# Kernel optimization log

Measured on AMD Instinct MI355X. Metric: run time of the kernel, lower is better.

Reference implementation:

```python
import jax, jax.numpy as jnp
import numpy as np

N, E, B = 20000, 160000, 64
NFEAT, NHID, HEADS, NCLASS = 128, 64, 16, 10
GAT_SLOPE = 0.2    # LeakyReLU inside GATv2 attention
OUT_SLOPE = 0.01   # torch.nn.functional.leaky_relu default
TEMPERATURE = 1.0


def _lrelu(x, slope):
    return jnp.where(x >= 0, x, slope * x)


def gatv2_conv(x, src, dst, Wl, bl, Wr, br, att, bias):
    # x: [N, Fin]; PyG GATv2Conv with share_weights=False, concat=False (mean over heads)
    xl = (x @ Wl + bl).reshape(N, HEADS, NHID)   # source-side transform
    xr = (x @ Wr + br).reshape(N, HEADS, NHID)   # target-side transform
    e = _lrelu(xl[src] + xr[dst], GAT_SLOPE)     # [E', H, C] per-edge pre-activation
    logit = jnp.einsum('ehc,hc->eh', e, att)     # [E', H]
    # segment softmax over incoming edges of each target node (self-loops guarantee >=1 edge)
    m = jax.ops.segment_max(logit, dst, num_segments=N)
    m = jnp.where(jnp.isfinite(m), m, 0.0)
    ex = jnp.exp(logit - m[dst])
    den = jax.ops.segment_sum(ex, dst, num_segments=N)
    alpha = ex / den[dst]                        # [E', H]
    out = jax.ops.segment_sum(alpha[:, :, None] * xl[src], dst, num_segments=N)  # [N, H, C]
    return out.mean(axis=1) + bias               # concat=False -> head average, then bias


def setup_inputs() -> dict:
    key = jax.random.key(0)
    ks = jax.random.split(key, 20)
    s = 0.05
    inp = {
        'x': jax.random.normal(ks[0], (N, NFEAT), dtype=jnp.float32),
        'edge_index': jax.random.randint(ks[1], (2, E), 0, N, dtype=jnp.int64)
            if jax.config.jax_enable_x64 else jax.random.randint(ks[1], (2, E), 0, N).astype(jnp.int32),
        'batch': jnp.sort(jax.random.randint(ks[2], (N,), 0, B)).astype(jnp.int32),
        # GATv2 layer 1
        'W1l': jax.random.normal(ks[3], (NFEAT, HEADS * NHID), dtype=jnp.float32) * s,
        'b1l': jnp.zeros((HEADS * NHID,), jnp.float32),
        'W1r': jax.random.normal(ks[4], (NFEAT, HEADS * NHID), dtype=jnp.float32) * s,
        'b1r': jnp.zeros((HEADS * NHID,), jnp.float32),
        'att1': jax.random.normal(ks[5], (HEADS, NHID), dtype=jnp.float32) * s,
        'bias1': jnp.zeros((NHID,), jnp.float32),
        # GATv2 layer 2
        'W2l': jax.random.normal(ks[6], (NHID, HEADS * NHID), dtype=jnp.float32) * s,
        'b2l': jnp.zeros((HEADS * NHID,), jnp.float32),
        'W2r': jax.random.normal(ks[7], (NHID, HEADS * NHID), dtype=jnp.float32) * s,
        'b2r': jnp.zeros((HEADS * NHID,), jnp.float32),
        'att2': jax.random.normal(ks[8], (HEADS, NHID), dtype=jnp.float32) * s,
        'bias2': jnp.zeros((NHID,), jnp.float32),
        # heads
        'Wc': jax.random.normal(ks[9], (NHID, NCLASS), dtype=jnp.float32) * s,
        'bc': jnp.zeros((NCLASS,), jnp.float32),
        'Wv': jax.random.normal(ks[10], (NHID, 1), dtype=jnp.float32) * s,
        'bv': jnp.zeros((1,), jnp.float32),
    }
    return inp


def reference(x, edge_index, batch, W1l, b1l, W1r, b1r, att1, bias1,
              W2l, b2l, W2r, b2r, att2, bias2, Wc, bc, Wv, bv):
    loop = jnp.arange(N, dtype=edge_index.dtype)  # PyG add_self_loops=True
    src = jnp.concatenate([edge_index[0], loop])
    dst = jnp.concatenate([edge_index[1], loop])

    h = _lrelu(gatv2_conv(x, src, dst, W1l, b1l, W1r, b1r, att1, bias1), OUT_SLOPE)
    h = _lrelu(gatv2_conv(h, src, dst, W2l, b2l, W2r, b2r, att2, bias2), OUT_SLOPE)
    # dropout p=0.0 -> identity

    sums = jax.ops.segment_sum(h, batch, num_segments=B)           # [B, NHID]
    cnt = jax.ops.segment_sum(jnp.ones((N,), h.dtype), batch, num_segments=B)
    pooled = sums / jnp.maximum(cnt, 1.0)[:, None]                 # global_mean_pool

    logits = (pooled @ Wc + bc) / TEMPERATURE                      # [B, NCLASS]
    log_var = pooled @ Wv + bv                                     # [B, 1]
    return (logits, log_var)
```

## Files before the change

### kernel.cpp

```cpp
#include <hip/hip_runtime.h>
#include <hip/hip_bf16.h>
#include <hip/hip_fp16.h>
#include <math.h>

#define NN   20000
#define EE   160000
#define NBAT 64
#define NF   128
#define NH   64
#define NHEAD 16
#define NCLS 10
#define ETOT (EE + NN)

typedef __attribute__((ext_vector_type(8))) _Float16 half8;
typedef __attribute__((ext_vector_type(2))) _Float16 h2v;
typedef __attribute__((ext_vector_type(4))) float f32x4;
typedef unsigned short ushort_t;

#if __has_builtin(__builtin_amdgcn_fdot2)
typedef __fp16 fdot2_t __attribute__((ext_vector_type(2)));
static __device__ __forceinline__ float dot2(h2v a, h2v b, float c) {
    return __builtin_amdgcn_fdot2(__builtin_bit_cast(fdot2_t, a),
                                  __builtin_bit_cast(fdot2_t, b), c, false);
}
#else
static __device__ __forceinline__ float dot2(h2v a, h2v b, float c) {
    return c + (float)a.x * (float)b.x + (float)a.y * (float)b.y;
}
#endif

__global__ void k_hist(const int* __restrict__ ei, int* __restrict__ deg) {
    int e = blockIdx.x * 256 + threadIdx.x;
    if (e < EE) atomicAdd(&deg[ei[EE + e]], 1);
}

__global__ void k_scan(const int* __restrict__ deg, int* __restrict__ rowptr,
                       int* __restrict__ cursor, int* __restrict__ csr) {
    const int T = 1024, PER = (NN + T - 1) / T;
    __shared__ int part[T];
    int t = threadIdx.x;
    int local[PER];
    int s = 0;
    #pragma unroll
    for (int i = 0; i < PER; ++i) {
        int idx = t * PER + i;
        int v = (idx < NN) ? deg[idx] : 0;
        local[i] = v; s += v;
    }
    part[t] = s;
    __syncthreads();
    for (int off = 1; off < T; off <<= 1) {
        int v = (t >= off) ? part[t - off] : 0;
        __syncthreads();
        part[t] += v;
        __syncthreads();
    }
    int ex = (t == 0) ? 0 : part[t - 1];
    #pragma unroll
    for (int i = 0; i < PER; ++i) {
        int idx = t * PER + i;
        if (idx < NN) {
            int base = ex + idx;
            rowptr[idx] = base;
            csr[base]   = idx;
            cursor[idx] = base + 1;
            ex += local[i];
        }
    }
    if (t == T - 1) rowptr[NN] = ex + NN;
}

__global__ void k_scatter(const int* __restrict__ ei, int* __restrict__ cursor,
                          int* __restrict__ csr) {
    int e = blockIdx.x * 256 + threadIdx.x;
    if (e >= EE) return;
    int s = ei[e], d = ei[EE + e];
    int pos = atomicAdd(&cursor[d], 1);
    csr[pos] = s;
}

__global__ void k_bounds(const int* __restrict__ batch, int* __restrict__ bstart) {
    int n = blockIdx.x * 256 + threadIdx.x;
    if (n >= NN) return;
    int b = batch[n];
    if (n == 0) for (int bb = 0; bb <= b; ++bb) bstart[bb] = 0;
    int bn = (n + 1 < NN) ? batch[n + 1] : NBAT;
    for (int bb = b + 1; bb <= bn; ++bb) bstart[bb] = n + 1;
}

__global__ void k_split_w4(
    const float* __restrict__ W0, _Float16* __restrict__ T0,
    const float* __restrict__ W1, _Float16* __restrict__ T1,
    const float* __restrict__ W2, _Float16* __restrict__ T2,
    const float* __restrict__ W3, _Float16* __restrict__ T3)
{
    const int z = blockIdx.y;
    const float* W; _Float16* T; int K;
    if      (z == 0) { W = W0; T = T0; K = NF; }
    else if (z == 1) { W = W1; T = T1; K = NF; }
    else if (z == 2) { W = W2; T = T2; K = NH; }
    else             { W = W3; T = T3; K = NH; }
    int idx = blockIdx.x * 256 + threadIdx.x;
    if (idx >= K * 1024) return;
    int k = idx >> 10, n = idx & 1023;
    T[n * K + k] = (_Float16)W[idx];
}


template<int K>
__global__ __launch_bounds__(256) void k_gemm_l1(
    const float* __restrict__ X, int M,
    const _Float16* __restrict__ Wt0, const float* __restrict__ b0, _Float16* __restrict__ O0,
    const _Float16* __restrict__ Wt1, const float* __restrict__ b1, _Float16* __restrict__ O1)
{
    const _Float16* Wt = blockIdx.z ? Wt1 : Wt0;
    const float*    bi = blockIdx.z ? b1 : b0;
    _Float16*       O  = blockIdx.z ? O1 : O0;

    const int r0 = blockIdx.x * 128;
    const int c0 = blockIdx.y * 128;

    __shared__ __align__(16) ushort_t SH[128 * 128];
    char* AsB = (char*)SH;
    char* WsB = (char*)SH + 16384;

    const int t = threadIdx.x;
    const int lane = t & 63;
    const int wv = t >> 6, wr = wv >> 1, wc = wv & 1;
    const int fr = lane & 15;
    const int k0 = (lane >> 4) * 8;

    f32x4 acc[4][4] = {};

    for (int kt = 0; kt < K; kt += 64) {
        #pragma unroll
        for (int p = 0; p < 4; ++p) {
            int idx = p * 256 + t;
            int m  = idx >> 3;
            int kc = (idx & 7) * 8;
            int gr = r0 + m;
            half8 hv = {};
            if (gr < M) {
                float4 v0 = *(const float4*)(X + (size_t)gr * K + kt + kc);
                float4 v1 = *(const float4*)(X + (size_t)gr * K + kt + kc + 4);
                hv[0] = (_Float16)v0.x; hv[1] = (_Float16)v0.y;
                hv[2] = (_Float16)v0.z; hv[3] = (_Float16)v0.w;
                hv[4] = (_Float16)v1.x; hv[5] = (_Float16)v1.y;
                hv[6] = (_Float16)v1.z; hv[7] = (_Float16)v1.w;
            }
            int sw = (m * 128 + kc * 2) ^ ((m & 7) << 4);
            *(uint4*)(AsB + sw) = __builtin_bit_cast(uint4, hv);
            uint4 wv4 = *(const uint4*)(Wt + (size_t)(c0 + m) * K + kt + kc);
            *(uint4*)(WsB + sw) = wv4;
        }
        __syncthreads();

        #pragma unroll
        for (int ks = 0; ks < 64; ks += 32) {
            half8 a[4], b[4];
            #pragma unroll
            for (int i = 0; i < 4; ++i) {
                int row = wr * 64 + i * 16 + fr;
                int off = (row * 128 + (ks + k0) * 2) ^ ((row & 7) << 4);
                a[i] = *(const half8*)(AsB + off);
            }
            #pragma unroll
            for (int j = 0; j < 4; ++j) {
                int col = wc * 64 + j * 16 + fr;
                int off = (col * 128 + (ks + k0) * 2) ^ ((col & 7) << 4);
                b[j] = *(const half8*)(WsB + off);
            }
            #pragma unroll
            for (int i = 0; i < 4; ++i)
                #pragma unroll
                for (int j = 0; j < 4; ++j)
                    acc[i][j] = __builtin_amdgcn_mfma_f32_16x16x32_f16(a[i], b[j], acc[i][j], 0, 0, 0);
        }
        __syncthreads();
    }

    float bj[4];
    #pragma unroll
    for (int j = 0; j < 4; ++j) bj[j] = bi[c0 + wc * 64 + j * 16 + fr];
    #pragma unroll
    for (int i = 0; i < 4; ++i) {
        #pragma unroll
        for (int r = 0; r < 4; ++r) {
            int row_l = wr * 64 + i * 16 + (lane >> 4) * 4 + r;
            int s = ((row_l >> 2) & 7) << 4;
            #pragma unroll
            for (int j = 0; j < 4; ++j) {
                int col_l = wc * 64 + j * 16 + fr;
                *(_Float16*)((char*)SH + ((row_l * 256 + col_l * 2) ^ s)) =
                    (_Float16)(acc[i][j][r] + bj[j]);
            }
        }
    }
    __syncthreads();
    #pragma unroll
    for (int it = 0; it < 8; ++it) {
        int idx = it * 256 + t;
        int row_l = idx >> 4, c16 = idx & 15;
        int gr = r0 + row_l;
        if (gr < M) {
            int s = ((row_l >> 2) & 7) << 4;
            uint4 v = *(const uint4*)((char*)SH + ((row_l * 256 + c16 * 16) ^ s));
            *(uint4*)(O + (size_t)gr * 1024 + c0 + c16 * 8) = v;
        }
    }
}

template<int K>
__global__ __launch_bounds__(256) void k_gemm_l2(
    const _Float16* __restrict__ A, int M,
    const _Float16* __restrict__ Wt0, const float* __restrict__ b0, _Float16* __restrict__ O0,
    const _Float16* __restrict__ Wt1, const float* __restrict__ b1, _Float16* __restrict__ O1)
{
    const _Float16* Wt = blockIdx.z ? Wt1 : Wt0;
    const float*    bi = blockIdx.z ? b1 : b0;
    _Float16*       O  = blockIdx.z ? O1 : O0;

    const int r0 = blockIdx.x * 128;
    const int c0 = blockIdx.y * 128;

    __shared__ __align__(16) ushort_t SH[128 * 128];
    char* AsB = (char*)SH;
    char* WsB = (char*)SH + 16384;

    const int t = threadIdx.x;
    const int lane = t & 63;
    const int wv = t >> 6, wr = wv >> 1, wc = wv & 1;
    const int fr = lane & 15;
    const int k0 = (lane >> 4) * 8;

    f32x4 acc[4][4] = {};

    #pragma unroll
    for (int p = 0; p < 4; ++p) {
        int idx = p * 256 + t;
        int m  = idx >> 3;
        int kc = (idx & 7) * 8;
        int gr = r0 + m;
        uint4 av = make_uint4(0, 0, 0, 0);
        if (gr < M) av = *(const uint4*)(A + (size_t)gr * K + kc);
        int sw = (m * 128 + kc * 2) ^ ((m & 7) << 4);
        *(uint4*)(AsB + sw) = av;
        uint4 wv4 = *(const uint4*)(Wt + (size_t)(c0 + m) * K + kc);
        *(uint4*)(WsB + sw) = wv4;
    }
    __syncthreads();

    #pragma unroll
    for (int ks = 0; ks < 64; ks += 32) {
        half8 a[4], b[4];
        #pragma unroll
        for (int i = 0; i < 4; ++i) {
            int row = wr * 64 + i * 16 + fr;
            int off = (row * 128 + (ks + k0) * 2) ^ ((row & 7) << 4);
            a[i] = *(const half8*)(AsB + off);
        }
        #pragma unroll
        for (int j = 0; j < 4; ++j) {
            int col = wc * 64 + j * 16 + fr;
            int off = (col * 128 + (ks + k0) * 2) ^ ((col & 7) << 4);
            b[j] = *(const half8*)(WsB + off);
        }
        #pragma unroll
        for (int i = 0; i < 4; ++i)
            #pragma unroll
            for (int j = 0; j < 4; ++j)
                acc[i][j] = __builtin_amdgcn_mfma_f32_16x16x32_f16(a[i], b[j], acc[i][j], 0, 0, 0);
    }
    __syncthreads();

    float bj[4];
    #pragma unroll
    for (int j = 0; j < 4; ++j) bj[j] = bi[c0 + wc * 64 + j * 16 + fr];
    #pragma unroll
    for (int i = 0; i < 4; ++i) {
        #pragma unroll
        for (int r = 0; r < 4; ++r) {
            int row_l = wr * 64 + i * 16 + (lane >> 4) * 4 + r;
            int s = ((row_l >> 2) & 7) << 4;
            #pragma unroll
            for (int j = 0; j < 4; ++j) {
                int col_l = wc * 64 + j * 16 + fr;
                *(_Float16*)((char*)SH + ((row_l * 256 + col_l * 2) ^ s)) =
                    (_Float16)(acc[i][j][r] + bj[j]);
            }
        }
    }
    __syncthreads();
    #pragma unroll
    for (int it = 0; it < 8; ++it) {
        int idx = it * 256 + t;
        int row_l = idx >> 4, c16 = idx & 15;
        int gr = r0 + row_l;
        if (gr < M) {
            int s = ((row_l >> 2) & 7) << 4;
            uint4 v = *(const uint4*)((char*)SH + ((row_l * 256 + c16 * 16) ^ s));
            *(uint4*)(O + (size_t)gr * 1024 + c0 + c16 * 8) = v;
        }
    }
}

static __device__ __forceinline__ float logit8(
    half8 a0, half8 a1, half8 xr0, half8 xr1, const h2v* att2)
{
    half8 t0 = a0 + xr0;
    half8 t1 = a1 + xr1;
    t0 = __builtin_elementwise_max(t0, t0 * (_Float16)0.2f);
    t1 = __builtin_elementwise_max(t1, t1 * (_Float16)0.2f);
    const h2v* p0 = (const h2v*)&t0;
    const h2v* p1 = (const h2v*)&t1;
    float lg = 0.f;
    #pragma unroll
    for (int j = 0; j < 4; ++j) lg = dot2(p0[j], att2[j], lg);
    #pragma unroll
    for (int j = 0; j < 4; ++j) lg = dot2(p1[j], att2[4 + j], lg);
    return lg;
}

template<int SPLIT>
__global__ __launch_bounds__(256) void k_attn(
    const _Float16* __restrict__ xl, const _Float16* __restrict__ xr,
    const float* __restrict__ att, const float* __restrict__ bias,
    const int* __restrict__ rowptr, const int* __restrict__ csr,
    float* __restrict__ hout, _Float16* __restrict__ h1out)
{
    const int wave = threadIdx.x >> 6;
    const int lane = threadIdx.x & 63;
    const int n = blockIdx.x * 4 + wave;
    if (n >= NN) return;
    const int h  = lane >> 2;
    const int cc = lane & 3;
    const int cb = h * NH + cc * 16;

    h2v att2[8];
    #pragma unroll
    for (int i = 0; i < 4; ++i) {
        float4 a = *(const float4*)(att + cb + i * 4);
        att2[i * 2 + 0] = h2v{(_Float16)a.x, (_Float16)a.y};
        att2[i * 2 + 1] = h2v{(_Float16)a.z, (_Float16)a.w};
    }
    const half8 xr0 = *(const half8*)(xr + (size_t)n * 1024 + cb);
    const half8 xr1 = *(const half8*)(xr + (size_t)n * 1024 + cb + 8);

    float acc[16];
    #pragma unroll
    for (int j = 0; j < 16; ++j) acc[j] = 0.f;
    float den = 0.f;

    const int e0 = rowptr[n], e1 = rowptr[n + 1];
    for (int e = e0; e < e1; e += 4) {
        int src[4];
        #pragma unroll
        for (int j = 0; j < 4; ++j) {
            int ee = e + j;
            src[j] = csr[(ee < e1) ? ee : (e1 - 1)];
        }
        half8 xa0[4], xa1[4];
        #pragma unroll
        for (int j = 0; j < 4; ++j) {
            const _Float16* p = xl + (size_t)src[j] * 1024 + cb;
            xa0[j] = *(const half8*)p;
            xa1[j] = *(const half8*)(p + 8);
        }
        #pragma unroll
        for (int j = 0; j < 4; ++j) {
            float lg = logit8(xa0[j], xa1[j], xr0, xr1, att2);
            lg += __shfl_xor(lg, 1);
            lg += __shfl_xor(lg, 2);
            float p = (e + j < e1) ? __expf(lg) : 0.f;
            den += p;
            const _Float16* va = (const _Float16*)&xa0[j];
            const _Float16* vb = (const _Float16*)&xa1[j];
            #pragma unroll
            for (int q = 0; q < 8; ++q) acc[q]     = fmaf((float)va[q], p, acc[q]);
            #pragma unroll
            for (int q = 0; q < 8; ++q) acc[8 + q] = fmaf((float)vb[q], p, acc[8 + q]);
        }
    }

    const float inv = 1.f / den;
    float v[16];
    #pragma unroll
    for (int j = 0; j < 16; ++j) v[j] = acc[j] * inv;
    #pragma unroll
    for (int mask = 4; mask <= 32; mask <<= 1)
        #pragma unroll
        for (int j = 0; j < 16; ++j) v[j] += __shfl_xor(v[j], mask);

    if (h == 0) {
        float bvv[16];
        #pragma unroll
        for (int i = 0; i < 4; ++i)
            *(float4*)(bvv + i * 4) = *(const float4*)(bias + cc * 16 + i * 4);
        float o[16];
        #pragma unroll
        for (int j = 0; j < 16; ++j) {
            float tt = v[j] * 0.0625f + bvv[j];
            o[j] = fmaxf(tt, 0.01f * tt);
        }
        if (SPLIT) {
            half8 o0, o1;
            #pragma unroll
            for (int j = 0; j < 8; ++j) { o0[j] = (_Float16)o[j]; o1[j] = (_Float16)o[8 + j]; }
            *(half8*)(h1out + (size_t)n * NH + cc * 16)     = o0;
            *(half8*)(h1out + (size_t)n * NH + cc * 16 + 8) = o1;
        } else {
            #pragma unroll
            for (int i = 0; i < 4; ++i)
                *(float4*)(hout + (size_t)n * NH + cc * 16 + i * 4) =
                    make_float4(o[i * 4], o[i * 4 + 1], o[i * 4 + 2], o[i * 4 + 3]);
        }
    }
}

#define PNODES 128
__global__ __launch_bounds__(256) void k_pool_partial(
    const float* __restrict__ h2buf, const int* __restrict__ batch,
    float* __restrict__ sums)
{
    const int n0 = blockIdx.x * PNODES;
    const int c = threadIdx.x & 63;
    const int r = threadIdx.x >> 6;
    const int nend = (n0 + PNODES < NN) ? n0 + PNODES : NN;
    float s = 0.f;
    int bcur = -1;
    for (int n = n0 + r; n < nend; n += 4) {
        int b = batch[n];
        if (b != bcur) {
            if (bcur >= 0) atomicAdd(&sums[bcur * NH + c], s);
            bcur = b; s = 0.f;
        }
        s += h2buf[(size_t)n * NH + c];
    }
    if (bcur >= 0) atomicAdd(&sums[bcur * NH + c], s);
}

__global__ void k_heads(const float* __restrict__ sums, const int* __restrict__ bstart,
                        const float* __restrict__ Wc, const float* __restrict__ bc,
                        const float* __restrict__ Wv, const float* __restrict__ bv,
                        float* __restrict__ out)
{
    const int b = blockIdx.x, c = threadIdx.x;
    const float cnt = (float)(bstart[b + 1] - bstart[b]);
    const float pooled = sums[b * NH + c] / fmaxf(cnt, 1.f);
    __shared__ float pl[NH];
    pl[c] = pooled;
    __syncthreads();
    if (c < NCLS) {
        float a = bc[c];
        for (int k = 0; k < NH; ++k) a = fmaf(pl[k], Wc[k * NCLS + c], a);
        out[b * NCLS + c] = a;
    } else if (c == NCLS) {
        float a = bv[0];
        for (int k = 0; k < NH; ++k) a = fmaf(pl[k], Wv[k], a);
        out[NBAT * NCLS + b] = a;
    }
}

extern "C" void kernel_launch(void* const* d_in, const int* in_sizes, int n_in,
                              void* d_out, int out_size, void* d_ws, size_t ws_size,
                              hipStream_t stream)
{
    const float* x     = (const float*)d_in[0];
    const int*   ei    = (const int*)  d_in[1];
    const int*   batch = (const int*)  d_in[2];
    const float* W1l = (const float*)d_in[3],  *b1l = (const float*)d_in[4];
    const float* W1r = (const float*)d_in[5],  *b1r = (const float*)d_in[6];
    const float* att1 = (const float*)d_in[7], *bias1 = (const float*)d_in[8];
    const float* W2l = (const float*)d_in[9],  *b2l = (const float*)d_in[10];
    const float* W2r = (const float*)d_in[11], *b2r = (const float*)d_in[12];
    const float* att2 = (const float*)d_in[13], *bias2 = (const float*)d_in[14];
    const float* Wc = (const float*)d_in[15],  *bc = (const float*)d_in[16];
    const float* Wv = (const float*)d_in[17],  *bv = (const float*)d_in[18];
    float* out = (float*)d_out;

    char* ws = (char*)d_ws;
    size_t off = 0;
    auto carve = [&](size_t bytes) {
        char* p = ws + off;
        off = (off + bytes + 255) & ~(size_t)255;
        return p;
    };
    _Float16* xl    = (_Float16*)carve((size_t)NN * 1024 * 2);
    _Float16* xr    = (_Float16*)carve((size_t)NN * 1024 * 2);
    float*    h2b   = (float*)carve((size_t)NN * NH * 4);
    float*    psums = (float*)carve((size_t)NBAT * NH * 4);
    _Float16* h1    = (_Float16*)carve((size_t)NN * NH * 2);
    _Float16* Wt1l  = (_Float16*)carve((size_t)1024 * NF * 2);
    _Float16* Wt1r  = (_Float16*)carve((size_t)1024 * NF * 2);
    _Float16* Wt2l  = (_Float16*)carve((size_t)1024 * NH * 2);
    _Float16* Wt2r  = (_Float16*)carve((size_t)1024 * NH * 2);
    int*      deg    = (int*)carve((size_t)NN * 4);
    int*      cursor = (int*)carve((size_t)NN * 4);
    int*      rowptr = (int*)carve((size_t)(NN + 1) * 4);
    int*      csr    = (int*)carve((size_t)ETOT * 4);
    int*      bstart = (int*)carve((size_t)(NBAT + 1) * 4);

    hipMemsetAsync(deg, 0, (size_t)NN * 4, stream);
    k_hist   <<<(EE + 255) / 256, 256, 0, stream>>>(ei, deg);
    k_scan   <<<1, 1024, 0, stream>>>(deg, rowptr, cursor, csr);
    k_scatter<<<(EE + 255) / 256, 256, 0, stream>>>(ei, cursor, csr);
    k_bounds <<<(NN + 255) / 256, 256, 0, stream>>>(batch, bstart);

    k_split_w4<<<dim3((NF * 1024 + 255) / 256, 4), 256, 0, stream>>>(
        W1l, Wt1l, W1r, Wt1r, W2l, Wt2l, W2r, Wt2r);

    const int MB = (NN + 127) / 128;
    k_gemm_l1<NF><<<dim3(MB, 8, 2), 256, 0, stream>>>(
        x, NN, Wt1l, b1l, xl, Wt1r, b1r, xr);
    k_attn<1><<<NN / 4, 256, 0, stream>>>(xl, xr, att1, bias1, rowptr, csr,
                                          (float*)nullptr, h1);
    k_gemm_l2<NH><<<dim3(MB, 8, 2), 256, 0, stream>>>(
        h1, NN, Wt2l, b2l, xl, Wt2r, b2r, xr);
    k_attn<0><<<NN / 4, 256, 0, stream>>>(xl, xr, att2, bias2, rowptr, csr,
                                          h2b, (_Float16*)nullptr);
    hipMemsetAsync(psums, 0, (size_t)NBAT * NH * 4, stream);
    k_pool_partial<<<(NN + PNODES - 1) / PNODES, 256, 0, stream>>>(h2b, batch, psums);
    k_heads<<<NBAT, NH, 0, stream>>>(psums, bstart, Wc, bc, Wv, bv, out);
}
```

Before: 357.4 us.

## Parallelize CSR scan, fuse bounds into histogram, fuse pooling into layer-2 attention

Replaces the single-block 1024-thread scan with a three-kernel multi-block scan (block scans, a serial prefix over block sums, then a final pass). Merges the batch-bounds kernel into the histogram kernel. Removes the layer-2 output buffer and the pooling kernel by having the second attention kernel atomically add each node's output straight into the per-graph sums. This trades many contended float atomics on 64x64 targets, about 20000 nodes times 64 channels, for dropping a 5 MB write/read and one launch, and it adds two scan launches.

Measured after the change: 758.1 us. +112.1%, slower.

```diff
diff --git a/kernel.cpp b/kernel.cpp
--- a/kernel.cpp
+++ b/kernel.cpp
@@ -12,6 +12,9 @@
 #define NCLS 10
 #define ETOT (EE + NN)
 
+#define SCAN_BLK 1024
+#define SCAN_NB  ((NN + SCAN_BLK - 1) / SCAN_BLK)
+
 typedef __attribute__((ext_vector_type(8))) _Float16 half8;
 typedef __attribute__((ext_vector_type(2))) _Float16 h2v;
 typedef __attribute__((ext_vector_type(4))) float f32x4;
@@ -29,45 +32,55 @@
 }
 #endif
 
-__global__ void k_hist(const int* __restrict__ ei, int* __restrict__ deg) {
-    int e = blockIdx.x * 256 + threadIdx.x;
-    if (e < EE) atomicAdd(&deg[ei[EE + e]], 1);
-}
-
-__global__ void k_scan(const int* __restrict__ deg, int* __restrict__ rowptr,
-                       int* __restrict__ cursor, int* __restrict__ csr) {
-    const int T = 1024, PER = (NN + T - 1) / T;
-    __shared__ int part[T];
-    int t = threadIdx.x;
-    int local[PER];
-    int s = 0;
-    #pragma unroll
-    for (int i = 0; i < PER; ++i) {
-        int idx = t * PER + i;
-        int v = (idx < NN) ? deg[idx] : 0;
-        local[i] = v; s += v;
-    }
-    part[t] = s;
+__global__ void k_hist_bounds(const int* __restrict__ ei, int* __restrict__ deg,
+                              const int* __restrict__ batch, int* __restrict__ bstart) {
+    int g = blockIdx.x * 256 + threadIdx.x;
+    if (g < EE) atomicAdd(&deg[ei[EE + g]], 1);
+    if (g < NN) {
+        int b = batch[g];
+        if (g == 0) for (int bb = 0; bb <= b; ++bb) bstart[bb] = 0;
+        int bn = (g + 1 < NN) ? batch[g + 1] : NBAT;
+        for (int bb = b + 1; bb <= bn; ++bb) bstart[bb] = g + 1;
+    }
+}
+
+__global__ void k_scanA(const int* __restrict__ deg, int* __restrict__ incl,
+                        int* __restrict__ bsum) {
+    __shared__ int sh[SCAN_BLK];
+    int t = threadIdx.x, idx = blockIdx.x * SCAN_BLK + t;
+    int v = (idx < NN) ? deg[idx] : 0;
+    sh[t] = v;
     __syncthreads();
-    for (int off = 1; off < T; off <<= 1) {
-        int v = (t >= off) ? part[t - off] : 0;
+    for (int off = 1; off < SCAN_BLK; off <<= 1) {
+        int u = (t >= off) ? sh[t - off] : 0;
         __syncthreads();
-        part[t] += v;
+        sh[t] += u;
         __syncthreads();
     }
-    int ex = (t == 0) ? 0 : part[t - 1];
-    #pragma unroll
-    for (int i = 0; i < PER; ++i) {
-        int idx = t * PER + i;
-        if (idx < NN) {
-            int base = ex + idx;
-            rowptr[idx] = base;
-            csr[base]   = idx;
-            cursor[idx] = base + 1;
-            ex += local[i];
-        }
-    }
-    if (t == T - 1) rowptr[NN] = ex + NN;
+    incl[idx] = sh[t];
+    if (t == SCAN_BLK - 1) bsum[blockIdx.x] = sh[t];
+}
+
+__global__ void k_scanB(const int* __restrict__ bsum, int* __restrict__ boff,
+                        int* __restrict__ rowptr) {
+    if (threadIdx.x == 0) {
+        int acc = 0;
+        for (int b = 0; b < SCAN_NB; ++b) { boff[b] = acc; acc += bsum[b]; }
+        rowptr[NN] = acc + NN;
+    }
+}
+
+__global__ void k_scanC(const int* __restrict__ deg, const int* __restrict__ incl,
+                        const int* __restrict__ boff, int* __restrict__ rowptr,
+                        int* __restrict__ cursor, int* __restrict__ csr) {
+    int idx = blockIdx.x * 256 + threadIdx.x;
+    if (idx >= NN) return;
+    int b = idx >> 10;
+    int excl = boff[b] + incl[idx] - deg[idx];
+    int base = excl + idx;
+    rowptr[idx] = base;
+    csr[base]   = idx;
+    cursor[idx] = base + 1;
 }
 
 __global__ void k_scatter(const int* __restrict__ ei, int* __restrict__ cursor,
@@ -77,15 +90,6 @@
     int s = ei[e], d = ei[EE + e];
     int pos = atomicAdd(&cursor[d], 1);
     csr[pos] = s;
-}
-
-__global__ void k_bounds(const int* __restrict__ batch, int* __restrict__ bstart) {
-    int n = blockIdx.x * 256 + threadIdx.x;
-    if (n >= NN) return;
-    int b = batch[n];
-    if (n == 0) for (int bb = 0; bb <= b; ++bb) bstart[bb] = 0;
-    int bn = (n + 1 < NN) ? batch[n + 1] : NBAT;
-    for (int bb = b + 1; bb <= bn; ++bb) bstart[bb] = n + 1;
 }
 
 __global__ void k_split_w4(
@@ -326,7 +330,8 @@
     const _Float16* __restrict__ xl, const _Float16* __restrict__ xr,
     const float* __restrict__ att, const float* __restrict__ bias,
     const int* __restrict__ rowptr, const int* __restrict__ csr,
-    float* __restrict__ hout, _Float16* __restrict__ h1out)
+    _Float16* __restrict__ h1out, const int* __restrict__ batch,
+    float* __restrict__ psums)
 {
     const int wave = threadIdx.x >> 6;
     const int lane = threadIdx.x & 63;
@@ -409,34 +414,11 @@
             *(half8*)(h1out + (size_t)n * NH + cc * 16)     = o0;
             *(half8*)(h1out + (size_t)n * NH + cc * 16 + 8) = o1;
         } else {
-            #pragma unroll
-            for (int i = 0; i < 4; ++i)
-                *(float4*)(hout + (size_t)n * NH + cc * 16 + i * 4) =
-                    make_float4(o[i * 4], o[i * 4 + 1], o[i * 4 + 2], o[i * 4 + 3]);
-        }
-    }
-}
-
-#define PNODES 128
-__global__ __launch_bounds__(256) void k_pool_partial(
-    const float* __restrict__ h2buf, const int* __restrict__ batch,
-    float* __restrict__ sums)
-{
-    const int n0 = blockIdx.x * PNODES;
-    const int c = threadIdx.x & 63;
-    const int r = threadIdx.x >> 6;
-    const int nend = (n0 + PNODES < NN) ? n0 + PNODES : NN;
-    float s = 0.f;
-    int bcur = -1;
-    for (int n = n0 + r; n < nend; n += 4) {
-        int b = batch[n];
-        if (b != bcur) {
-            if (bcur >= 0) atomicAdd(&sums[bcur * NH + c], s);
-            bcur = b; s = 0.f;
-        }
-        s += h2buf[(size_t)n * NH + c];
-    }
-    if (bcur >= 0) atomicAdd(&sums[bcur * NH + c], s);
+            float* ps = psums + batch[n] * NH + cc * 16;
+            #pragma unroll
+            for (int j = 0; j < 16; ++j) atomicAdd(&ps[j], o[j]);
+        }
+    }
 }
 
 __global__ void k_heads(const float* __restrict__ sums, const int* __restrict__ bstart,
@@ -487,7 +469,6 @@
     };
     _Float16* xl    = (_Float16*)carve((size_t)NN * 1024 * 2);
     _Float16* xr    = (_Float16*)carve((size_t)NN * 1024 * 2);
-    float*    h2b   = (float*)carve((size_t)NN * NH * 4);
     float*    psums = (float*)carve((size_t)NBAT * NH * 4);
     _Float16* h1    = (_Float16*)carve((size_t)NN * NH * 2);
     _Float16* Wt1l  = (_Float16*)carve((size_t)1024 * NF * 2);
@@ -495,16 +476,22 @@
     _Float16* Wt2l  = (_Float16*)carve((size_t)1024 * NH * 2);
     _Float16* Wt2r  = (_Float16*)carve((size_t)1024 * NH * 2);
     int*      deg    = (int*)carve((size_t)NN * 4);
+    int*      incl   = (int*)carve((size_t)SCAN_NB * SCAN_BLK * 4);
+    int*      bsum   = (int*)carve((size_t)SCAN_NB * 4);
+    int*      boff   = (int*)carve((size_t)SCAN_NB * 4);
     int*      cursor = (int*)carve((size_t)NN * 4);
     int*      rowptr = (int*)carve((size_t)(NN + 1) * 4);
     int*      csr    = (int*)carve((size_t)ETOT * 4);
     int*      bstart = (int*)carve((size_t)(NBAT + 1) * 4);
 
     hipMemsetAsync(deg, 0, (size_t)NN * 4, stream);
-    k_hist   <<<(EE + 255) / 256, 256, 0, stream>>>(ei, deg);
-    k_scan   <<<1, 1024, 0, stream>>>(deg, rowptr, cursor, csr);
+    hipMemsetAsync(psums, 0, (size_t)NBAT * NH * 4, stream);
+
+    k_hist_bounds<<<(EE + 255) / 256, 256, 0, stream>>>(ei, deg, batch, bstart);
+    k_scanA<<<SCAN_NB, SCAN_BLK, 0, stream>>>(deg, incl, bsum);
+    k_scanB<<<1, 64, 0, stream>>>(bsum, boff, rowptr);
+    k_scanC<<<(NN + 255) / 256, 256, 0, stream>>>(deg, incl, boff, rowptr, cursor, csr);
     k_scatter<<<(EE + 255) / 256, 256, 0, stream>>>(ei, cursor, csr);
-    k_bounds <<<(NN + 255) / 256, 256, 0, stream>>>(batch, bstart);
 
     k_split_w4<<<dim3((NF * 1024 + 255) / 256, 4), 256, 0, stream>>>(
         W1l, Wt1l, W1r, Wt1r, W2l, Wt2l, W2r, Wt2r);
@@ -513,12 +500,10 @@
     k_gemm_l1<NF><<<dim3(MB, 8, 2), 256, 0, stream>>>(
         x, NN, Wt1l, b1l, xl, Wt1r, b1r, xr);
     k_attn<1><<<NN / 4, 256, 0, stream>>>(xl, xr, att1, bias1, rowptr, csr,
-                                          (float*)nullptr, h1);
+                                          h1, batch, psums);
     k_gemm_l2<NH><<<dim3(MB, 8, 2), 256, 0, stream>>>(
         h1, NN, Wt2l, b2l, xl, Wt2r, b2r, xr);
     k_attn<0><<<NN / 4, 256, 0, stream>>>(xl, xr, att2, bias2, rowptr, csr,
-                                          h2b, (_Float16*)nullptr);
-    hipMemsetAsync(psums, 0, (size_t)NBAT * NH * 4, stream);
-    k_pool_partial<<<(NN + PNODES - 1) / PNODES, 256, 0, stream>>>(h2b, batch, psums);
+                                          (_Float16*)nullptr, batch, psums);
     k_heads<<<NBAT, NH, 0, stream>>>(psums, bstart, Wc, bc, Wv, bv, out);
 }
```
